# Optimization experiments

Measured on AMD Instinct MI355X. Metric: run time of the kernel, lower is better.

Reference implementation:

```python
import jax, jax.numpy as jnp
import numpy as np

N, IN, HID, HEADS, HC, E, K = 50000, 512, 256, 8, 32, 600000, 4
EPS = 1e-5


def _gcn(h_in, W, b, src, dst):
    # PyG GCNConv: add self-loops, symmetric normalization, linear + bias
    h = h_in @ W  # [N, out]
    loop = jnp.arange(N)
    s = jnp.concatenate([src, loop])
    d = jnp.concatenate([dst, loop])
    deg = jax.ops.segment_sum(jnp.ones(s.shape[0], h.dtype), d, num_segments=N)
    dinv = jnp.where(deg > 0, jax.lax.rsqrt(deg), 0.0)
    msg = h[s] * (dinv[s] * dinv[d])[:, None]
    return jax.ops.segment_sum(msg, d, num_segments=N) + b


def _gat(h_in, W, a_src, a_dst, b, src, dst):
    # PyG GATConv: self-loops, LeakyReLU(0.2) logits, per-dst softmax, concat heads
    loop = jnp.arange(N)
    s = jnp.concatenate([src, loop])
    d = jnp.concatenate([dst, loop])
    h = (h_in @ W).reshape(N, HEADS, HC)
    e = jax.nn.leaky_relu((h * a_src).sum(-1)[s] + (h * a_dst).sum(-1)[d], 0.2)  # [E', H]
    m = jax.ops.segment_max(e, d, num_segments=N)  # every node has a self-loop
    ex = jnp.exp(e - m[d])
    alpha = ex / jax.ops.segment_sum(ex, d, num_segments=N)[d]
    out = jax.ops.segment_sum(h[s] * alpha[:, :, None], d, num_segments=N)  # [N, H, C]
    return out.reshape(N, HID) + b


def _ln(h, g, bta):
    mu = h.mean(-1, keepdims=True)
    var = ((h - mu) ** 2).mean(-1, keepdims=True)
    return (h - mu) * jax.lax.rsqrt(var + EPS) * g + bta


def _forward(x, style, stress, params, edges):
    (gW0, gb0, gW1, gb1, gW2, gb2, aW, aas, aad, ab, lg, lb, fW1, fb1, fW2, fb2) = params
    outs = []
    for k in range(K):
        src, dst = edges[k][0], edges[k][1]
        h = jax.nn.relu(_gcn(x, gW0[k], gb0[k], src, dst))
        h = jax.nn.relu(_gcn(h, gW1[k], gb1[k], src, dst))
        h = jax.nn.relu(_gcn(h, gW2[k], gb2[k], src, dst))
        h = _gat(h, aW[k], aas[k], aad[k], ab[k], src, dst)
        outs.append(_ln(h, lg[k], lb[k]))
    ctx = jnp.concatenate([style, stress], axis=-1)
    w = jax.nn.softmax(jnp.tanh(ctx @ fW1 + fb1) @ fW2 + fb2, axis=-1)  # [N, K]
    stacked = jnp.stack(outs, axis=1)  # [N, K, HID]
    return jnp.einsum('nk,nkd->nd', w, stacked)


def setup_inputs() -> dict:
    key = jax.random.key(0)
    ks = jax.random.split(key, 16)
    rn = lambda k, shape, s=0.05: jax.random.normal(k, shape, jnp.float32) * s
    return {
        "x": rn(ks[0], (N, IN), 1.0),
        "style_features": rn(ks[1], (N, HID), 1.0),
        "stress_features": rn(ks[2], (N, HID), 1.0),
        "edge_index0": jax.random.randint(ks[3], (2, E), 0, N),
        "edge_index1": jax.random.randint(ks[4], (2, E), 0, N),
        "edge_index2": jax.random.randint(ks[5], (2, E), 0, N),
        "edge_index3": jax.random.randint(ks[6], (2, E), 0, N),
        "gcn_W0": rn(ks[7], (K, IN, HID)),
        "gcn_b0": jnp.zeros((K, HID), jnp.float32),
        "gcn_W1": rn(ks[8], (K, HID, HID)),
        "gcn_b1": jnp.zeros((K, HID), jnp.float32),
        "gcn_W2": rn(ks[9], (K, HID, HID)),
        "gcn_b2": jnp.zeros((K, HID), jnp.float32),
        "gat_W": rn(ks[10], (K, HID, HID)),
        "gat_a_src": rn(ks[11], (K, HEADS, HC), 0.1),
        "gat_a_dst": rn(ks[12], (K, HEADS, HC), 0.1),
        "gat_b": jnp.zeros((K, HID), jnp.float32),
        "ln_g": jnp.ones((K, HID), jnp.float32),
        "ln_b": jnp.zeros((K, HID), jnp.float32),
        "fus_W1": rn(ks[13], (2 * HID, HID)),
        "fus_b1": jnp.zeros((HID,), jnp.float32),
        "fus_W2": rn(ks[14], (HID, K)),
        "fus_b2": jnp.zeros((K,), jnp.float32),
    }


def reference(x, edge_index0, edge_index1, edge_index2, edge_index3, style_features, stress_features, gcn_W0, gcn_b0, gcn_W1, gcn_b1, gcn_W2, gcn_b2, gat_W, gat_a_src, gat_a_dst, gat_b, ln_g, ln_b, fus_W1, fus_b1, fus_W2, fus_b2):
    params = (gcn_W0, gcn_b0, gcn_W1, gcn_b1, gcn_W2, gcn_b2, gat_W, gat_a_src, gat_a_dst, gat_b, ln_g, ln_b, fus_W1, fus_b1, fus_W2, fus_b2)
    edges = (edge_index0, edge_index1, edge_index2, edge_index3)
    return _forward(x, style_features, stress_features, params, edges)
```

## Files before the change

kernel.cpp:

```cpp
#include <hip/hip_runtime.h>
#include <hip/hip_bf16.h>
#include <cstdint>

#define N_NODES 50000
#define IN_DIM  512
#define HID     256
#define NEDGE   600000
#define TOPO    4
#define DEGMAX  96

typedef __attribute__((ext_vector_type(4))) float floatx4;
typedef _Float16 half4 __attribute__((ext_vector_type(4)));
typedef _Float16 half8 __attribute__((ext_vector_type(8)));

static __device__ __forceinline__ unsigned f2ord(float f) {
  unsigned b = __float_as_uint(f);
  return (b & 0x80000000u) ? ~b : (b | 0x80000000u);
}
static __device__ __forceinline__ float ord2f(unsigned u) {
  unsigned b = (u & 0x80000000u) ? (u & 0x7fffffffu) : ~u;
  return __uint_as_float(b);
}

__global__ void conv_f2h_kernel(const float* __restrict__ src, _Float16* __restrict__ dst, int n4) {
  int i = blockIdx.x * 256 + threadIdx.x;
  if (i < n4) {
    float4 v = ((const float4*)src)[i];
    half4 h;
    h[0] = (_Float16)v.x; h[1] = (_Float16)v.y; h[2] = (_Float16)v.z; h[3] = (_Float16)v.w;
    ((half4*)dst)[i] = h;
  }
}

__global__ void conv_ctx_kernel(const float* __restrict__ style, const float* __restrict__ stress,
                                _Float16* __restrict__ dst) {
  int i = blockIdx.x * 256 + threadIdx.x;
  if (i >= N_NODES * 128) return;
  int n = i >> 7, c4 = i & 127;
  int c = c4 * 4;
  const float* s = (c < 256) ? (style + (size_t)n * 256 + c) : (stress + (size_t)n * 256 + (c - 256));
  float4 v = *(const float4*)s;
  half4 h;
  h[0] = (_Float16)v.x; h[1] = (_Float16)v.y; h[2] = (_Float16)v.z; h[3] = (_Float16)v.w;
  ((half4*)(dst + (size_t)n * 512))[c4] = h;
}

#define WT_FUS 0
#define WT_G0  131072
#define WT_G1  655360
#define WT_G2  917504
#define WT_AW  1179648
#define WT_TOT 1441792
__global__ void wconv_all_kernel(const float* __restrict__ fW1, const float* __restrict__ gW0,
                                 const float* __restrict__ gW1, const float* __restrict__ gW2,
                                 const float* __restrict__ aW, _Float16* __restrict__ wt) {
  int idx = blockIdx.x * 256 + threadIdx.x;
  if (idx >= WT_TOT) return;
  const float* src;
  int local, sh;
  if (idx < WT_G0) { src = fW1; sh = 9; local = idx; }
  else if (idx < WT_G1) { int r = idx - WT_G0; src = gW0 + (size_t)(r >> 17) * 131072; sh = 9; local = r & 131071; }
  else if (idx < WT_G2) { int r = idx - WT_G1; src = gW1 + (size_t)(r >> 16) * 65536; sh = 8; local = r & 65535; }
  else if (idx < WT_AW) { int r = idx - WT_G2; src = gW2 + (size_t)(r >> 16) * 65536; sh = 8; local = r & 65535; }
  else { int r = idx - WT_AW; src = aW + (size_t)(r >> 16) * 65536; sh = 8; local = r & 65535; }
  int n = local >> sh;
  int kd = local & ((1 << sh) - 1);
  wt[idx] = (_Float16)src[(size_t)kd * 256 + n];
}

template <int KD>
__global__ __launch_bounds__(256, 3) void gemm_f16_kernel(
    const _Float16* __restrict__ A, const _Float16* __restrict__ Wt0,
    const float* __restrict__ bias, _Float16* __restrict__ C0, int M, int mode,
    const float* __restrict__ scale, int wt_stride, int c_stride) {
  constexpr int NIT = KD / 32;
  const _Float16* Wt = Wt0 + (size_t)blockIdx.y * wt_stride;
  _Float16* C = C0 + (size_t)blockIdx.y * c_stride;
  __shared__ __align__(16) _Float16 As[2][2048];
  const int tid = threadIdx.x;
  const int lane = tid & 63;
  const int wv = tid >> 6;
  const int mr = lane & 15;
  const int q = (lane >> 4) & 3;
  const int r0 = blockIdx.x * 64;

  int arow = r0 + ((tid >> 6) * 16) + (tid & 15);
  if (arow > M - 1) arow = M - 1;
  const _Float16* pa = A + (size_t)arow * KD + ((tid >> 4) & 3) * 8;
  const _Float16* pb[4];
#pragma unroll
  for (int t = 0; t < 4; ++t)
    pb[t] = Wt + (size_t)((wv * 4 + t) * 16 + mr) * KD + q * 8;

  floatx4 acc[4][4];
#pragma unroll
  for (int g = 0; g < 4; ++g)
#pragma unroll
    for (int t = 0; t < 4; ++t) acc[g][t] = (floatx4){0.f, 0.f, 0.f, 0.f};

  half8 a0, a1, b0[4], b1[4];
  a0 = *(const half8*)pa; pa += 32;
#pragma unroll
  for (int t = 0; t < 4; ++t) { b0[t] = *(const half8*)pb[t]; pb[t] += 32; }
  *(half8*)&As[0][(unsigned)tid * 8] = a0;
  if (NIT > 1) { a1 = *(const half8*)pa; pa += 32; }
  __syncthreads();

#pragma unroll 1
  for (int it = 0; it < NIT; it += 2) {
    if (it + 1 < NIT) {
      *(half8*)&As[1][(unsigned)tid * 8] = a1;
#pragma unroll
      for (int t = 0; t < 4; ++t) { b1[t] = *(const half8*)pb[t]; pb[t] += 32; }
      if (it + 2 < NIT) { a0 = *(const half8*)pa; pa += 32; }
    }
    {
      half8 af[4];
#pragma unroll
      for (int g = 0; g < 4; ++g) af[g] = *(const half8*)&As[0][(g * 64 + lane) * 8];
#pragma unroll
      for (int g = 0; g < 4; ++g)
#pragma unroll
        for (int t = 0; t < 4; ++t)
          acc[g][t] = __builtin_amdgcn_mfma_f32_16x16x32_f16(b0[t], af[g], acc[g][t], 0, 0, 0);
    }
    if (it + 1 < NIT) {
      __syncthreads();
      if (it + 2 < NIT) {
        *(half8*)&As[0][(unsigned)tid * 8] = a0;
#pragma unroll
        for (int t = 0; t < 4; ++t) { b0[t] = *(const half8*)pb[t]; pb[t] += 32; }
        if (it + 3 < NIT) { a1 = *(const half8*)pa; pa += 32; }
      }
      half8 af[4];
#pragma unroll
      for (int g = 0; g < 4; ++g) af[g] = *(const half8*)&As[1][(g * 64 + lane) * 8];
#pragma unroll
      for (int g = 0; g < 4; ++g)
#pragma unroll
        for (int t = 0; t < 4; ++t)
          acc[g][t] = __builtin_amdgcn_mfma_f32_16x16x32_f16(b1[t], af[g], acc[g][t], 0, 0, 0);
      if (it + 2 < NIT) __syncthreads();
    }
  }

  float sv[4];
#pragma unroll
  for (int g = 0; g < 4; ++g) {
    int row = r0 + g * 16 + mr;
    sv[g] = (scale && row < M) ? scale[row] : 1.f;
  }
#pragma unroll
  for (int t = 0; t < 4; ++t) {
    int c0 = (wv * 4 + t) * 16 + q * 4;
    float4 bv;
    if (bias) bv = *(const float4*)&bias[c0];
    else { bv.x = 0.f; bv.y = 0.f; bv.z = 0.f; bv.w = 0.f; }
#pragma unroll
    for (int g = 0; g < 4; ++g) {
      int row = r0 + g * 16 + mr;
      if (row < M) {
        half4 o;
#pragma unroll
        for (int r = 0; r < 4; ++r) {
          float v = acc[g][t][r] + (&bv.x)[r];
          if (mode == 1) v = tanhf(v);
          v *= sv[g];
          o[r] = (_Float16)v;
        }
        *(half4*)&C[(size_t)row * HID + c0] = o;
      }
    }
  }
}

__global__ void zero_int_kernel(int* p, int n, unsigned* gmax) {
  int i = blockIdx.x * 256 + threadIdx.x;
  if (i < n) p[i] = 0;
  if (blockIdx.x == 0 && threadIdx.x < 8) gmax[threadIdx.x] = 0u;
}
__global__ void fill_kernel(const int* __restrict__ src, const int* __restrict__ dst,
                            int* __restrict__ cur, int* __restrict__ csr_src, int n) {
  int i = blockIdx.x * 256 + threadIdx.x;
  if (i < n) {
    int d = dst[i];
    int slot = atomicAdd(&cur[d], 1);
    if (slot < DEGMAX) csr_src[(size_t)d * DEGMAX + slot] = src[i];
  }
}
__global__ void dinv_kernel(const int* __restrict__ deg, float* __restrict__ dinv, int n) {
  int i = blockIdx.x * 256 + threadIdx.x;
  if (i < n) dinv[i] = rsqrtf((float)(deg[i] + 1));
}

template <int PRESCALED>
__global__ __launch_bounds__(256) void gcn_agg_kernel(
    const _Float16* __restrict__ hlin, const int* __restrict__ deg,
    const int* __restrict__ csr_src, const float* __restrict__ dinv,
    const float* __restrict__ bias, _Float16* __restrict__ out) {
  int w = (int)((blockIdx.x * blockDim.x + threadIdx.x) >> 6);
  int lane = threadIdx.x & 63;
  if (w >= N_NODES) return;
  float dv = dinv[w];
  half4 hv = ((const half4*)(hlin + (size_t)w * HID))[lane];
  float selfs = PRESCALED ? 1.f : dv;
  float A0 = (float)hv[0] * selfs, A1 = (float)hv[1] * selfs,
        A2 = (float)hv[2] * selfs, A3 = (float)hv[3] * selfs;
  float B0 = 0.f, B1 = 0.f, B2 = 0.f, B3 = 0.f;
  float C0 = 0.f, C1 = 0.f, C2 = 0.f, C3 = 0.f;
  float D0 = 0.f, D1 = 0.f, D2 = 0.f, D3 = 0.f;
  int dg = deg[w];
  if (dg > DEGMAX) dg = DEGMAX;
  const int* sp = csr_src + (size_t)w * DEGMAX;
  int s = 0;
  if (dg >= 4) {
    int4 iv = *(const int4*)sp;
    half4 p0 = ((const half4*)(hlin + (size_t)iv.x * HID))[lane];
    half4 p1 = ((const half4*)(hlin + (size_t)iv.y * HID))[lane];
    half4 p2 = ((const half4*)(hlin + (size_t)iv.z * HID))[lane];
    half4 p3 = ((const half4*)(hlin + (size_t)iv.w * HID))[lane];
    float e0 = 1.f, e1 = 1.f, e2 = 1.f, e3 = 1.f;
    if (!PRESCALED) { e0 = dinv[iv.x]; e1 = dinv[iv.y]; e2 = dinv[iv.z]; e3 = dinv[iv.w]; }
    for (s = 4; s + 4 <= dg; s += 4) {
      int4 nx = *(const int4*)(sp + s);
      half4 q0 = ((const half4*)(hlin + (size_t)nx.x * HID))[lane];
      half4 q1 = ((const half4*)(hlin + (size_t)nx.y * HID))[lane];
      half4 q2 = ((const half4*)(hlin + (size_t)nx.z * HID))[lane];
      half4 q3 = ((const half4*)(hlin + (size_t)nx.w * HID))[lane];
      float f0 = 1.f, f1 = 1.f, f2 = 1.f, f3 = 1.f;
      if (!PRESCALED) { f0 = dinv[nx.x]; f1 = dinv[nx.y]; f2 = dinv[nx.z]; f3 = dinv[nx.w]; }
      if (PRESCALED) {
        A0 += (float)p0[0]; A1 += (float)p0[1]; A2 += (float)p0[2]; A3 += (float)p0[3];
        B0 += (float)p1[0]; B1 += (float)p1[1]; B2 += (float)p1[2]; B3 += (float)p1[3];
        C0 += (float)p2[0]; C1 += (float)p2[1]; C2 += (float)p2[2]; C3 += (float)p2[3];
        D0 += (float)p3[0]; D1 += (float)p3[1]; D2 += (float)p3[2]; D3 += (float)p3[3];
      } else {
        A0 += (float)p0[0] * e0; A1 += (float)p0[1] * e0; A2 += (float)p0[2] * e0; A3 += (float)p0[3] * e0;
        B0 += (float)p1[0] * e1; B1 += (float)p1[1] * e1; B2 += (float)p1[2] * e1; B3 += (float)p1[3] * e1;
        C0 += (float)p2[0] * e2; C1 += (float)p2[1] * e2; C2 += (float)p2[2] * e2; C3 += (float)p2[3] * e2;
        D0 += (float)p3[0] * e3; D1 += (float)p3[1] * e3; D2 += (float)p3[2] * e3; D3 += (float)p3[3] * e3;
      }
      p0 = q0; p1 = q1; p2 = q2; p3 = q3;
      e0 = f0; e1 = f1; e2 = f2; e3 = f3;
    }
    if (PRESCALED) {
      A0 += (float)p0[0]; A1 += (float)p0[1]; A2 += (float)p0[2]; A3 += (float)p0[3];
      B0 += (float)p1[0]; B1 += (float)p1[1]; B2 += (float)p1[2]; B3 += (float)p1[3];
      C0 += (float)p2[0]; C1 += (float)p2[1]; C2 += (float)p2[2]; C3 += (float)p2[3];
      D0 += (float)p3[0]; D1 += (float)p3[1]; D2 += (float)p3[2]; D3 += (float)p3[3];
    } else {
      A0 += (float)p0[0] * e0; A1 += (float)p0[1] * e0; A2 += (float)p0[2] * e0; A3 += (float)p0[3] * e0;
      B0 += (float)p1[0] * e1; B1 += (float)p1[1] * e1; B2 += (float)p1[2] * e1; B3 += (float)p1[3] * e1;
      C0 += (float)p2[0] * e2; C1 += (float)p2[1] * e2; C2 += (float)p2[2] * e2; C3 += (float)p2[3] * e2;
      D0 += (float)p3[0] * e3; D1 += (float)p3[1] * e3; D2 += (float)p3[2] * e3; D3 += (float)p3[3] * e3;
    }
  }
  for (; s < dg; ++s) {
    int sc = sp[s];
    float nr = PRESCALED ? 1.f : dinv[sc];
    half4 v = ((const half4*)(hlin + (size_t)sc * HID))[lane];
    A0 += (float)v[0] * nr; A1 += (float)v[1] * nr;
    A2 += (float)v[2] * nr; A3 += (float)v[3] * nr;
  }
  float4 b = ((const float4*)bias)[lane];
  half4 r;
  r[0] = (_Float16)fmaxf((A0 + B0 + C0 + D0) * dv + b.x, 0.f);
  r[1] = (_Float16)fmaxf((A1 + B1 + C1 + D1) * dv + b.y, 0.f);
  r[2] = (_Float16)fmaxf((A2 + B2 + C2 + D2) * dv + b.z, 0.f);
  r[3] = (_Float16)fmaxf((A3 + B3 + C3 + D3) * dv + b.w, 0.f);
  ((half4*)(out + (size_t)w * HID))[lane] = r;
}

__global__ __launch_bounds__(256) void gat_prep_kernel(
    const _Float16* __restrict__ hlin, const float* __restrict__ a_src,
    const float* __restrict__ a_dst, float* __restrict__ asad) {
  int w = (int)((blockIdx.x * blockDim.x + threadIdx.x) >> 6);
  int lane = threadIdx.x & 63;
  if (w >= N_NODES) return;
  half4 h = ((const half4*)(hlin + (size_t)w * HID))[lane];
  float4 s4 = ((const float4*)a_src)[lane];
  float4 d4 = ((const float4*)a_dst)[lane];
  float hx = h[0], hy = h[1], hz = h[2], hw = h[3];
  float ps = hx * s4.x + hy * s4.y + hz * s4.z + hw * s4.w;
  float pd = hx * d4.x + hy * d4.y + hz * d4.z + hw * d4.w;
  for (int o = 1; o < 8; o <<= 1) { ps += __shfl_xor(ps, o, 64); pd += __shfl_xor(pd, o, 64); }
  if ((lane & 7) == 0) {
    int hh = lane >> 3;
    asad[(size_t)w * 16 + hh] = ps;
    asad[(size_t)w * 16 + 8 + hh] = pd;
  }
}

__global__ __launch_bounds__(256) void gmax_kernel(const float* __restrict__ asad,
                                                   unsigned* __restrict__ gmax) {
  int t = threadIdx.x;
  int h = t & 7;
  float m = -1e30f;
  for (int n = blockIdx.x * 32 + (t >> 3); n < N_NODES; n += gridDim.x * 32)
    m = fmaxf(m, asad[(size_t)n * 16 + h]);
  m = fmaxf(m, __shfl_xor(m, 8, 64));
  m = fmaxf(m, __shfl_xor(m, 16, 64));
  m = fmaxf(m, __shfl_xor(m, 32, 64));
  if ((t & 63) < 8) atomicMax(&gmax[h], f2ord(m));
}

static __device__ __forceinline__ float lrelu(float e) {
  return e > 0.f ? e : 0.2f * e;
}

__global__ __launch_bounds__(256) void gat_agg_kernel(
    const _Float16* __restrict__ hlin, const int* __restrict__ deg,
    const int* __restrict__ csr_src, const float* __restrict__ asad,
    const unsigned* __restrict__ gmax, const float* __restrict__ bias,
    const float* __restrict__ lng, const float* __restrict__ lnb,
    const float* __restrict__ wsel, int kk, float* __restrict__ dout) {
  int w = (int)((blockIdx.x * blockDim.x + threadIdx.x) >> 6);
  int lane = threadIdx.x & 63;
  if (w >= N_NODES) return;
  int head = lane >> 3;
  int e7 = lane & 7;
  int gsel = lane >> 4;
  float ad_d = asad[(size_t)w * 16 + 8 + head];
  float m = lrelu(ord2f(gmax[head]) + ad_d);
  float e_self = lrelu(asad[(size_t)w * 16 + head] + ad_d);
  float ad_e = __shfl(ad_d, e7 << 3, 64);
  float m_e = __shfl(m, e7 << 3, 64);
  int dg = deg[w];
  if (dg > DEGMAX) dg = DEGMAX;
  const int* sp = csr_src + (size_t)w * DEGMAX;
  float lA = __expf(e_self - m), lB = 0.f, lC = 0.f, lD = 0.f;
  half4 hv = ((const half4*)(hlin + (size_t)w * HID))[lane];
  float A0 = (float)hv[0] * lA, A1 = (float)hv[1] * lA,
        A2 = (float)hv[2] * lA, A3 = (float)hv[3] * lA;
  float B0 = 0.f, B1 = 0.f, B2 = 0.f, B3 = 0.f;
  float C0 = 0.f, C1 = 0.f, C2 = 0.f, C3 = 0.f;
  float D0 = 0.f, D1 = 0.f, D2 = 0.f, D3 = 0.f;
  int ng = (dg + 3) >> 2;
  int4 iv;
  if (ng) iv = *(const int4*)sp;
  for (int gi = 0; gi < ng; ++gi) {
    int s4 = gi << 2;
    int rem = dg - s4;
    bool tail = rem < 4;
    if (tail) {
      if (rem < 2) iv.y = iv.x;
      if (rem < 3) iv.z = iv.x;
      iv.w = iv.x;
    }
    int nsel = gsel == 0 ? iv.x : gsel == 1 ? iv.y : gsel == 2 ? iv.z : iv.w;
    float av = asad[(size_t)nsel * 16 + e7];
    half4 v0 = ((const half4*)(hlin + (size_t)iv.x * HID))[lane];
    half4 v1 = ((const half4*)(hlin + (size_t)iv.y * HID))[lane];
    half4 v2 = ((const half4*)(hlin + (size_t)iv.z * HID))[lane];
    half4 v3 = ((const half4*)(hlin + (size_t)iv.w * HID))[lane];
    int4 nx = iv;
    if (gi + 1 < ng) nx = *(const int4*)(sp + s4 + 4);
    float ve = __expf(lrelu(av + ad_e) - m_e);
    float w0 = __shfl(ve, head, 64);
    float w1 = __shfl(ve, 16 + head, 64);
    float w2 = __shfl(ve, 32 + head, 64);
    float w3 = __shfl(ve, 48 + head, 64);
    if (tail) {
      if (rem < 2) w1 = 0.f;
      if (rem < 3) w2 = 0.f;
      w3 = 0.f;
    }
    lA += w0; lB += w1; lC += w2; lD += w3;
    A0 += (float)v0[0] * w0; A1 += (float)v0[1] * w0; A2 += (float)v0[2] * w0; A3 += (float)v0[3] * w0;
    B0 += (float)v1[0] * w1; B1 += (float)v1[1] * w1; B2 += (float)v1[2] * w1; B3 += (float)v1[3] * w1;
    C0 += (float)v2[0] * w2; C1 += (float)v2[1] * w2; C2 += (float)v2[2] * w2; C3 += (float)v2[3] * w2;
    D0 += (float)v3[0] * w3; D1 += (float)v3[1] * w3; D2 += (float)v3[2] * w3; D3 += (float)v3[3] * w3;
    iv = nx;
  }
  float inv = 1.f / (lA + lB + lC + lD);
  float4 b = ((const float4*)bias)[lane];
  float vx = (A0 + B0 + C0 + D0) * inv + b.x;
  float vy = (A1 + B1 + C1 + D1) * inv + b.y;
  float vz = (A2 + B2 + C2 + D2) * inv + b.z;
  float vw = (A3 + B3 + C3 + D3) * inv + b.w;
  float ssum = vx + vy + vz + vw;
  for (int o = 1; o < 64; o <<= 1) ssum += __shfl_xor(ssum, o, 64);
  float mu = ssum * (1.f / HID);
  float dx = vx - mu, dy = vy - mu, dz = vz - mu, dw = vw - mu;
  float qq = dx * dx + dy * dy + dz * dz + dw * dw;
  for (int o = 1; o < 64; o <<= 1) qq += __shfl_xor(qq, o, 64);
  float rs = rsqrtf(qq * (1.f / HID) + 1e-5f);
  float4 g4 = ((const float4*)lng)[lane];
  float4 b4 = ((const float4*)lnb)[lane];
  float wk = wsel[(size_t)w * 4 + kk];
  float4 r;
  r.x = (dx * rs * g4.x + b4.x) * wk;
  r.y = (dy * rs * g4.y + b4.y) * wk;
  r.z = (dz * rs * g4.z + b4.z) * wk;
  r.w = (dw * rs * g4.w + b4.w) * wk;
  float4* dp = (float4*)(dout + (size_t)w * HID) + lane;
  if (kk == 0) {
    *dp = r;
  } else {
    float4 old = *dp;
    old.x += r.x; old.y += r.y; old.z += r.z; old.w += r.w;
    *dp = old;
  }
}

__global__ __launch_bounds__(256) void fusw_kernel(
    const _Float16* __restrict__ t, const float* __restrict__ W2,
    const float* __restrict__ b2, float* __restrict__ wout) {
  int w = (int)((blockIdx.x * blockDim.x + threadIdx.x) >> 6);
  int lane = threadIdx.x & 63;
  if (w >= N_NODES) return;
  half4 t4h = ((const half4*)(t + (size_t)w * HID))[lane];
  float tx = t4h[0], ty = t4h[1], tz = t4h[2], tw = t4h[3];
  int c = lane * 4;
  float4 w0 = ((const float4*)W2)[c + 0];
  float4 w1 = ((const float4*)W2)[c + 1];
  float4 w2 = ((const float4*)W2)[c + 2];
  float4 w3 = ((const float4*)W2)[c + 3];
  float p0 = tx * w0.x + ty * w1.x + tz * w2.x + tw * w3.x;
  float p1 = tx * w0.y + ty * w1.y + tz * w2.y + tw * w3.y;
  float p2 = tx * w0.z + ty * w1.z + tz * w2.z + tw * w3.z;
  float p3 = tx * w0.w + ty * w1.w + tz * w2.w + tw * w3.w;
  for (int o = 1; o < 64; o <<= 1) {
    p0 += __shfl_xor(p0, o, 64); p1 += __shfl_xor(p1, o, 64);
    p2 += __shfl_xor(p2, o, 64); p3 += __shfl_xor(p3, o, 64);
  }
  if (lane == 0) {
    p0 += b2[0]; p1 += b2[1]; p2 += b2[2]; p3 += b2[3];
    float mx = fmaxf(fmaxf(p0, p1), fmaxf(p2, p3));
    float e0 = __expf(p0 - mx), e1 = __expf(p1 - mx), e2 = __expf(p2 - mx), e3 = __expf(p3 - mx);
    float inv = 1.f / (e0 + e1 + e2 + e3);
    float4 r; r.x = e0 * inv; r.y = e1 * inv; r.z = e2 * inv; r.w = e3 * inv;
    ((float4*)wout)[w] = r;
  }
}

extern "C" void kernel_launch(void* const* d_in, const int* in_sizes, int n_in,
                              void* d_out, int out_size, void* d_ws, size_t ws_size,
                              hipStream_t stream) {
  const float* x      = (const float*)d_in[0];
  const float* style  = (const float*)d_in[1];
  const float* stress = (const float*)d_in[2];
  const int* edges[4] = {(const int*)d_in[3], (const int*)d_in[4],
                         (const int*)d_in[5], (const int*)d_in[6]};
  const float* gW0 = (const float*)d_in[7];
  const float* gb0 = (const float*)d_in[8];
  const float* gW1 = (const float*)d_in[9];
  const float* gb1 = (const float*)d_in[10];
  const float* gW2 = (const float*)d_in[11];
  const float* gb2 = (const float*)d_in[12];
  const float* aW  = (const float*)d_in[13];
  const float* aas = (const float*)d_in[14];
  const float* aad = (const float*)d_in[15];
  const float* ab  = (const float*)d_in[16];
  const float* lg  = (const float*)d_in[17];
  const float* lb  = (const float*)d_in[18];
  const float* fW1 = (const float*)d_in[19];
  const float* fb1 = (const float*)d_in[20];
  const float* fW2 = (const float*)d_in[21];
  const float* fb2 = (const float*)d_in[22];
  float* out = (float*)d_out;
  (void)in_sizes; (void)n_in; (void)out_size;

  char* wsp = (char*)d_ws;
  size_t off = 0;
  auto alloc = [&](size_t bytes) -> void* {
    void* p = wsp + off;
    off += (bytes + 255) & ~(size_t)255;
    return p;
  };
  auto al = [](size_t b) { return (b + 255) & ~(size_t)255; };

  const size_t sz_hact = (size_t)N_NODES * HID * 2;
  const size_t sz_xh   = (size_t)N_NODES * IN_DIM * 2;
  const size_t sz_csr  = (size_t)N_NODES * DEGMAX * 4;
  const size_t sz_hlin0 = (size_t)4 * N_NODES * HID * 2;

  const size_t fixed = al(sz_hact) * 2 + al(sz_xh) + al((size_t)WT_TOT * 2) +
                       al((size_t)N_NODES * 16) + al((size_t)N_NODES * 4) * 2 +
                       al((size_t)N_NODES * 64) + al(256);
  const size_t need_hoist = fixed + al(sz_csr) + al(sz_hlin0);
  const bool hoist = ws_size >= need_hoist;

  _Float16* h_act = (_Float16*)alloc(sz_hact);
  _Float16* h_lin = (_Float16*)alloc(sz_hact);
  _Float16* x_h   = (_Float16*)alloc(sz_xh);
  _Float16* wtall = (_Float16*)alloc((size_t)WT_TOT * 2);
  float* wsel = (float*)alloc((size_t)N_NODES * 16);
  float* dinv = (float*)alloc((size_t)N_NODES * 4);
  int* cur = (int*)alloc((size_t)N_NODES * 4);
  float* asad = (float*)alloc((size_t)N_NODES * 64);
  unsigned* gmax = (unsigned*)alloc(256);
  _Float16* ctx_h;
  int* csr_src;
  _Float16* h_lin0 = nullptr;
  if (hoist) {
    csr_src = (int*)alloc(sz_csr);
    char* region = (char*)alloc(sz_hlin0);
    ctx_h = (_Float16*)region;
    h_lin0 = (_Float16*)region;
  } else {
    char* shared_region = (char*)alloc(sz_xh);
    ctx_h = (_Float16*)shared_region;
    csr_src = (int*)shared_region;
  }

  dim3 blk(256);
  const int nodeWaveBlocks = N_NODES / 4;
  const int nBlocksN = (N_NODES + 255) / 256;
  const int nBlocksE = (NEDGE + 255) / 256;
  const int gemmBlocks = (N_NODES + 63) / 64;

  conv_f2h_kernel<<<(N_NODES * IN_DIM / 4 + 255) / 256, blk, 0, stream>>>(x, x_h, N_NODES * IN_DIM / 4);
  conv_ctx_kernel<<<(N_NODES * 128 + 255) / 256, blk, 0, stream>>>(style, stress, ctx_h);
  wconv_all_kernel<<<(WT_TOT + 255) / 256, blk, 0, stream>>>(fW1, gW0, gW1, gW2, aW, wtall);

  gemm_f16_kernel<512><<<gemmBlocks, blk, 0, stream>>>(ctx_h, wtall + WT_FUS, fb1, h_lin,
                                                       N_NODES, 1, nullptr, 0, 0);
  fusw_kernel<<<nodeWaveBlocks, blk, 0, stream>>>(h_lin, fW2, fb2, wsel);

  if (hoist) {
    gemm_f16_kernel<512><<<dim3(gemmBlocks, 4), blk, 0, stream>>>(
        x_h, wtall + WT_G0, nullptr, h_lin0, N_NODES, 0, nullptr,
        131072, N_NODES * HID);
  }

  for (int k = 0; k < TOPO; ++k) {
    const int* srcp = edges[k];
    const int* dstp = edges[k] + NEDGE;
    zero_int_kernel<<<nBlocksN, blk, 0, stream>>>(cur, N_NODES, gmax);
    fill_kernel<<<nBlocksE, blk, 0, stream>>>(srcp, dstp, cur, csr_src, NEDGE);
    dinv_kernel<<<nBlocksN, blk, 0, stream>>>(cur, dinv, N_NODES);

    if (hoist) {
      gcn_agg_kernel<0><<<nodeWaveBlocks, blk, 0, stream>>>(
          h_lin0 + (size_t)k * N_NODES * HID, cur, csr_src, dinv,
          gb0 + (size_t)k * HID, h_act);
    } else {
      gemm_f16_kernel<512><<<gemmBlocks, blk, 0, stream>>>(
          x_h, wtall + WT_G0 + (size_t)k * 131072, nullptr, h_lin, N_NODES, 0, dinv, 0, 0);
      gcn_agg_kernel<1><<<nodeWaveBlocks, blk, 0, stream>>>(h_lin, cur, csr_src, dinv,
                                                            gb0 + (size_t)k * HID, h_act);
    }
    gemm_f16_kernel<256><<<gemmBlocks, blk, 0, stream>>>(
        h_act, wtall + WT_G1 + (size_t)k * 65536, nullptr, h_lin, N_NODES, 0, dinv, 0, 0);
    gcn_agg_kernel<1><<<nodeWaveBlocks, blk, 0, stream>>>(h_lin, cur, csr_src, dinv,
                                                          gb1 + (size_t)k * HID, h_act);
    gemm_f16_kernel<256><<<gemmBlocks, blk, 0, stream>>>(
        h_act, wtall + WT_G2 + (size_t)k * 65536, nullptr, h_lin, N_NODES, 0, dinv, 0, 0);
    gcn_agg_kernel<1><<<nodeWaveBlocks, blk, 0, stream>>>(h_lin, cur, csr_src, dinv,
                                                          gb2 + (size_t)k * HID, h_act);
    gemm_f16_kernel<256><<<gemmBlocks, blk, 0, stream>>>(
        h_act, wtall + WT_AW + (size_t)k * 65536, nullptr, h_lin, N_NODES, 0, nullptr, 0, 0);
    gat_prep_kernel<<<nodeWaveBlocks, blk, 0, stream>>>(h_lin, aas + (size_t)k * HID,
                                                        aad + (size_t)k * HID, asad);
    gmax_kernel<<<64, blk, 0, stream>>>(asad, gmax);
    gat_agg_kernel<<<nodeWaveBlocks, blk, 0, stream>>>(h_lin, cur, csr_src, asad, gmax,
                                                       ab + (size_t)k * HID,
                                                       lg + (size_t)k * HID,
                                                       lb + (size_t)k * HID,
                                                       wsel, k, out);
  }
}
```

Baseline: 1.902 ms.

## Drop LDS staging in f16 GEMM and interleave batched weight blocks

The GEMM no longer stages A tiles through shared memory with barriers. Each lane loads its own A fragments directly from global memory into registers, double-buffered, and the K loop is fully unrolled. The hoisted batched GEMM now folds the batch index into the low bits of blockIdx.x, so blocks that share a row tile but use different weights run close together and can reuse A in cache. This removes LDS traffic and syncs but makes each A element be loaded four times per block (once per wave) from global memory or L2, and raises register pressure.

```diff
diff --git a/kernel.cpp b/kernel.cpp
--- a/kernel.cpp
+++ b/kernel.cpp
@@ -72,21 +72,26 @@
 __global__ __launch_bounds__(256, 3) void gemm_f16_kernel(
     const _Float16* __restrict__ A, const _Float16* __restrict__ Wt0,
     const float* __restrict__ bias, _Float16* __restrict__ C0, int M, int mode,
-    const float* __restrict__ scale, int wt_stride, int c_stride) {
+    const float* __restrict__ scale, int wt_stride, int c_stride, int bsh) {
   constexpr int NIT = KD / 32;
-  const _Float16* Wt = Wt0 + (size_t)blockIdx.y * wt_stride;
-  _Float16* C = C0 + (size_t)blockIdx.y * c_stride;
-  __shared__ __align__(16) _Float16 As[2][2048];
+  const int batch = blockIdx.x & ((1 << bsh) - 1);
+  const int tile = blockIdx.x >> bsh;
+  const _Float16* Wt = Wt0 + (size_t)batch * wt_stride;
+  _Float16* C = C0 + (size_t)batch * c_stride;
   const int tid = threadIdx.x;
   const int lane = tid & 63;
   const int wv = tid >> 6;
   const int mr = lane & 15;
   const int q = (lane >> 4) & 3;
-  const int r0 = blockIdx.x * 64;
-
-  int arow = r0 + ((tid >> 6) * 16) + (tid & 15);
-  if (arow > M - 1) arow = M - 1;
-  const _Float16* pa = A + (size_t)arow * KD + ((tid >> 4) & 3) * 8;
+  const int r0 = tile * 64;
+
+  const _Float16* pa[4];
+#pragma unroll
+  for (int g = 0; g < 4; ++g) {
+    int row = r0 + g * 16 + mr;
+    if (row > M - 1) row = M - 1;
+    pa[g] = A + (size_t)row * KD + q * 8;
+  }
   const _Float16* pb[4];
 #pragma unroll
   for (int t = 0; t < 4; ++t)
@@ -98,49 +103,43 @@
 #pragma unroll
     for (int t = 0; t < 4; ++t) acc[g][t] = (floatx4){0.f, 0.f, 0.f, 0.f};
 
-  half8 a0, a1, b0[4], b1[4];
-  a0 = *(const half8*)pa; pa += 32;
-#pragma unroll
-  for (int t = 0; t < 4; ++t) { b0[t] = *(const half8*)pb[t]; pb[t] += 32; }
-  *(half8*)&As[0][(unsigned)tid * 8] = a0;
-  if (NIT > 1) { a1 = *(const half8*)pa; pa += 32; }
-  __syncthreads();
-
-#pragma unroll 1
+  half8 a0[4], b0[4], a1[4], b1[4];
+#pragma unroll
+  for (int g = 0; g < 4; ++g) a0[g] = *(const half8*)(pa[g]);
+#pragma unroll
+  for (int t = 0; t < 4; ++t) b0[t] = *(const half8*)(pb[t]);
+  if (NIT > 1) {
+#pragma unroll
+    for (int g = 0; g < 4; ++g) a1[g] = *(const half8*)(pa[g] + 32);
+#pragma unroll
+    for (int t = 0; t < 4; ++t) b1[t] = *(const half8*)(pb[t] + 32);
+  }
+
+#pragma unroll
   for (int it = 0; it < NIT; it += 2) {
+#pragma unroll
+    for (int g = 0; g < 4; ++g)
+#pragma unroll
+      for (int t = 0; t < 4; ++t)
+        acc[g][t] = __builtin_amdgcn_mfma_f32_16x16x32_f16(b0[t], a0[g], acc[g][t], 0, 0, 0);
+    if (it + 2 < NIT) {
+#pragma unroll
+      for (int g = 0; g < 4; ++g) a0[g] = *(const half8*)(pa[g] + (it + 2) * 32);
+#pragma unroll
+      for (int t = 0; t < 4; ++t) b0[t] = *(const half8*)(pb[t] + (it + 2) * 32);
+    }
     if (it + 1 < NIT) {
-      *(half8*)&As[1][(unsigned)tid * 8] = a1;
-#pragma unroll
-      for (int t = 0; t < 4; ++t) { b1[t] = *(const half8*)pb[t]; pb[t] += 32; }
-      if (it + 2 < NIT) { a0 = *(const half8*)pa; pa += 32; }
-    }
-    {
-      half8 af[4];
-#pragma unroll
-      for (int g = 0; g < 4; ++g) af[g] = *(const half8*)&As[0][(g * 64 + lane) * 8];
 #pragma unroll
       for (int g = 0; g < 4; ++g)
 #pragma unroll
         for (int t = 0; t < 4; ++t)
-          acc[g][t] = __builtin_amdgcn_mfma_f32_16x16x32_f16(b0[t], af[g], acc[g][t], 0, 0, 0);
-    }
-    if (it + 1 < NIT) {
-      __syncthreads();
-      if (it + 2 < NIT) {
-        *(half8*)&As[0][(unsigned)tid * 8] = a0;
-#pragma unroll
-        for (int t = 0; t < 4; ++t) { b0[t] = *(const half8*)pb[t]; pb[t] += 32; }
-        if (it + 3 < NIT) { a1 = *(const half8*)pa; pa += 32; }
+          acc[g][t] = __builtin_amdgcn_mfma_f32_16x16x32_f16(b1[t], a1[g], acc[g][t], 0, 0, 0);
+      if (it + 3 < NIT) {
+#pragma unroll
+        for (int g = 0; g < 4; ++g) a1[g] = *(const half8*)(pa[g] + (it + 3) * 32);
+#pragma unroll
+        for (int t = 0; t < 4; ++t) b1[t] = *(const half8*)(pb[t] + (it + 3) * 32);
       }
-      half8 af[4];
-#pragma unroll
-      for (int g = 0; g < 4; ++g) af[g] = *(const half8*)&As[1][(g * 64 + lane) * 8];
-#pragma unroll
-      for (int g = 0; g < 4; ++g)
-#pragma unroll
-        for (int t = 0; t < 4; ++t)
-          acc[g][t] = __builtin_amdgcn_mfma_f32_16x16x32_f16(b1[t], af[g], acc[g][t], 0, 0, 0);
-      if (it + 2 < NIT) __syncthreads();
     }
   }
 
@@ -515,13 +514,13 @@
   wconv_all_kernel<<<(WT_TOT + 255) / 256, blk, 0, stream>>>(fW1, gW0, gW1, gW2, aW, wtall);
 
   gemm_f16_kernel<512><<<gemmBlocks, blk, 0, stream>>>(ctx_h, wtall + WT_FUS, fb1, h_lin,
-                                                       N_NODES, 1, nullptr, 0, 0);
+                                                       N_NODES, 1, nullptr, 0, 0, 0);
   fusw_kernel<<<nodeWaveBlocks, blk, 0, stream>>>(h_lin, fW2, fb2, wsel);
 
   if (hoist) {
-    gemm_f16_kernel<512><<<dim3(gemmBlocks, 4), blk, 0, stream>>>(
+    gemm_f16_kernel<512><<<gemmBlocks * 4, blk, 0, stream>>>(
         x_h, wtall + WT_G0, nullptr, h_lin0, N_NODES, 0, nullptr,
-        131072, N_NODES * HID);
+        131072, N_NODES * HID, 2);
   }
 
   for (int k = 0; k < TOPO; ++k) {
@@ -537,20 +536,20 @@
           gb0 + (size_t)k * HID, h_act);
     } else {
       gemm_f16_kernel<512><<<gemmBlocks, blk, 0, stream>>>(
-          x_h, wtall + WT_G0 + (size_t)k * 131072, nullptr, h_lin, N_NODES, 0, dinv, 0, 0);
+          x_h, wtall + WT_G0 + (size_t)k * 131072, nullptr, h_lin, N_NODES, 0, dinv, 0, 0, 0);
       gcn_agg_kernel<1><<<nodeWaveBlocks, blk, 0, stream>>>(h_lin, cur, csr_src, dinv,
                                                             gb0 + (size_t)k * HID, h_act);
     }
     gemm_f16_kernel<256><<<gemmBlocks, blk, 0, stream>>>(
-        h_act, wtall + WT_G1 + (size_t)k * 65536, nullptr, h_lin, N_NODES, 0, dinv, 0, 0);
+        h_act, wtall + WT_G1 + (size_t)k * 65536, nullptr, h_lin, N_NODES, 0, dinv, 0, 0, 0);
     gcn_agg_kernel<1><<<nodeWaveBlocks, blk, 0, stream>>>(h_lin, cur, csr_src, dinv,
                                                           gb1 + (size_t)k * HID, h_act);
     gemm_f16_kernel<256><<<gemmBlocks, blk, 0, stream>>>(
-        h_act, wtall + WT_G2 + (size_t)k * 65536, nullptr, h_lin, N_NODES, 0, dinv, 0, 0);
+        h_act, wtall + WT_G2 + (size_t)k * 65536, nullptr, h_lin, N_NODES, 0, dinv, 0, 0, 0);
     gcn_agg_kernel<1><<<nodeWaveBlocks, blk, 0, stream>>>(h_lin, cur, csr_src, dinv,
                                                           gb2 + (size_t)k * HID, h_act);
     gemm_f16_kernel<256><<<gemmBlocks, blk, 0, stream>>>(
-        h_act, wtall + WT_AW + (size_t)k * 65536, nullptr, h_lin, N_NODES, 0, nullptr, 0, 0);
+        h_act, wtall + WT_AW + (size_t)k * 65536, nullptr, h_lin, N_NODES, 0, nullptr, 0, 0, 0);
     gat_prep_kernel<<<nodeWaveBlocks, blk, 0, stream>>>(h_lin, aas + (size_t)k * HID,
                                                         aad + (size_t)k * HID, asad);
     gmax_kernel<<<64, blk, 0, stream>>>(asad, gmax);
```

Measured after the change: 2.200 ms. 1.16x slower.
